# Kernel optimization log

Hardware: AMD Instinct MI355X
Metric: run time of the kernel (lower is better)

## Reference

```python
import jax, jax.numpy as jnp
import numpy as np

ALPHA, BETA, LMBD, GAMMA = 0.0005, 1.0, 1.0, 1.0
MARGIN, THRES = 100.0, 0.5
EPS = 1e-7


def _bce(p, t):
    p = jnp.clip(p, EPS, 1.0 - EPS)
    return -jnp.mean(t * jnp.log(p) + (1.0 - t) * jnp.log1p(-p))


def setup_inputs() -> dict:
    key = jax.random.key(0)
    ks = jax.random.split(key, 9)
    B, T, D, C = 16, 2048, 2048, 100
    return {
        "score_act": jax.random.uniform(ks[0], (B, C), jnp.float32),
        "score_bkg": jax.random.uniform(ks[1], (B, C), jnp.float32),
        "feat_act": jax.random.normal(ks[2], (B, T, D), jnp.float32),
        "feat_bkg": jax.random.normal(ks[3], (B, T, D), jnp.float32),
        "label": jax.random.uniform(ks[4], (B, C), jnp.float32),
        "gt": jax.random.uniform(ks[5], (B, T, C), jnp.float32),
        "sup_cas": jax.random.uniform(ks[6], (B, T, C), jnp.float32),
        "cas_s": jax.random.uniform(ks[7], (B, T, C), jnp.float32),
        "cas_t": jax.random.uniform(ks[8], (B, T, C), jnp.float32),
    }


def reference(score_act, score_bkg, feat_act, feat_bkg, label, gt, sup_cas, cas_s, cas_t):
    # classification BCE against normalized multi-label target
    label_n = label / jnp.sum(label, axis=1, keepdims=True)
    loss_cls = _bce(score_act, label_n)

    # background BCE against uniform 1/C target
    C = label.shape[1]
    loss_be = _bce(score_bkg, jnp.full_like(label, 1.0 / C))

    # uncertainty modeling: feature-magnitude margin loss
    act_norm = jnp.linalg.norm(jnp.mean(feat_act, axis=1), axis=1)  # [B]
    bkg_norm = jnp.linalg.norm(jnp.mean(feat_bkg, axis=1), axis=1)  # [B]
    loss_act = jnp.maximum(MARGIN - act_norm, 0.0)
    loss_um = jnp.mean((loss_act + bkg_norm) ** 2)

    # balanced_ce, vectorized over (batch, class): mean of L2 norms over time
    # for (i,j) slices that contain at least one positive snippet
    pmask = (gt > THRES).astype(sup_cas.dtype)            # [B,T,C]
    norms = jnp.linalg.norm(sup_cas - pmask, axis=1)      # [B,C]
    valid = jnp.sum(pmask, axis=1) > 0                    # [B,C]
    count = jnp.maximum(jnp.sum(valid), 1).astype(norms.dtype)
    loss_sup = jnp.sum(jnp.where(valid, norms, 0.0)) / count

    # student/teacher CAS MSE
    loss_st = jnp.mean((cas_s - cas_t) ** 2)

    loss_total = (loss_cls + ALPHA * loss_um + BETA * loss_be
                  + LMBD * loss_sup + GAMMA * loss_st)
    return jnp.stack([loss_total, loss_cls, loss_be, loss_um, loss_sup, loss_st])
```

## Files before the change

kernel.cpp:

```cpp
#include <hip/hip_runtime.h>
#include <cmath>

constexpr int B = 16, T = 2048, D = 2048, C = 100;
#define EPS_F 1e-7f

__global__ void colsum_kernel(const float* __restrict__ feat, float* __restrict__ out,
                              int rows_per_chunk) {
    const int b = blockIdx.z;
    const int d0 = (blockIdx.x * blockDim.x + threadIdx.x) * 4;
    const int t0 = blockIdx.y * rows_per_chunk;
    float4 acc = make_float4(0.f, 0.f, 0.f, 0.f);
    const float* base = feat + ((size_t)b * T + t0) * D + d0;
    for (int t = 0; t < rows_per_chunk; ++t) {
        float4 v = *reinterpret_cast<const float4*>(base + (size_t)t * D);
        acc.x += v.x; acc.y += v.y; acc.z += v.z; acc.w += v.w;
    }
    float* o = out + b * D + d0;
    atomicAdd(o + 0, acc.x);
    atomicAdd(o + 1, acc.y);
    atomicAdd(o + 2, acc.z);
    atomicAdd(o + 3, acc.w);
}

__global__ void sup_kernel(const float* __restrict__ gt, const float* __restrict__ sup,
                           float* __restrict__ sumsq, float* __restrict__ cnt,
                           int rows_per_chunk) {
    const int b = blockIdx.y;
    const int c = threadIdx.x;
    const int t0 = blockIdx.x * rows_per_chunk;
    if (c >= C) return;
    float acc = 0.f, pc = 0.f;
    size_t base = ((size_t)b * T + t0) * C + c;
    for (int t = 0; t < rows_per_chunk; ++t) {
        float g = gt[base + (size_t)t * C];
        float s = sup[base + (size_t)t * C];
        float m = (g > 0.5f) ? 1.f : 0.f;
        float d = s - m;
        acc += d * d;
        pc += m;
    }
    atomicAdd(&sumsq[b * C + c], acc);
    atomicAdd(&cnt[b * C + c], pc);
}

__global__ void st_kernel(const float4* __restrict__ s, const float4* __restrict__ t,
                          float* __restrict__ acc, int n4) {
    int idx = blockIdx.x * blockDim.x + threadIdx.x;
    int stride = gridDim.x * blockDim.x;
    float local = 0.f;
    for (int i = idx; i < n4; i += stride) {
        float4 a = s[i], b4 = t[i];
        float dx = a.x - b4.x, dy = a.y - b4.y, dz = a.z - b4.z, dw = a.w - b4.w;
        local += dx * dx + dy * dy + dz * dz + dw * dw;
    }
    for (int off = 32; off; off >>= 1) local += __shfl_down(local, off, 64);
    __shared__ float wsum[4];
    int lane = threadIdx.x & 63, wv = threadIdx.x >> 6;
    if (lane == 0) wsum[wv] = local;
    __syncthreads();
    if (threadIdx.x == 0) {
        atomicAdd(acc, wsum[0] + wsum[1] + wsum[2] + wsum[3]);
    }
}

__device__ __forceinline__ float block_reduce256(float v, float* sdata) {
    int tid = threadIdx.x;
    sdata[tid] = v;
    __syncthreads();
    for (int s = 128; s > 0; s >>= 1) {
        if (tid < s) sdata[tid] += sdata[tid + s];
        __syncthreads();
    }
    float r = sdata[0];
    __syncthreads();
    return r;
}

__global__ void final_kernel(const float* __restrict__ score_act,
                             const float* __restrict__ score_bkg,
                             const float* __restrict__ label,
                             const float* __restrict__ colsum_act,
                             const float* __restrict__ colsum_bkg,
                             const float* __restrict__ sup_sumsq,
                             const float* __restrict__ sup_cnt,
                             const float* __restrict__ st_acc,
                             float* __restrict__ out) {
    __shared__ float sdata[256];
    __shared__ float rowsum[B];
    __shared__ float an[B], bn[B];
    const int tid = threadIdx.x;
    const int N = B * C;

    if (tid < B) rowsum[tid] = 0.f;
    __syncthreads();
    for (int i = tid; i < N; i += 256) atomicAdd(&rowsum[i / C], label[i]);
    __syncthreads();

    float lc = 0.f;
    for (int i = tid; i < N; i += 256) {
        float tgt = label[i] / rowsum[i / C];
        float p = fminf(fmaxf(score_act[i], EPS_F), 1.f - EPS_F);
        lc -= tgt * logf(p) + (1.f - tgt) * log1pf(-p);
    }
    float loss_cls = block_reduce256(lc, sdata) / (float)N;

    float lb = 0.f;
    const float u = 1.f / (float)C;
    for (int i = tid; i < N; i += 256) {
        float p = fminf(fmaxf(score_bkg[i], EPS_F), 1.f - EPS_F);
        lb -= u * logf(p) + (1.f - u) * log1pf(-p);
    }
    float loss_be = block_reduce256(lb, sdata) / (float)N;

    const float invT = 1.f / (float)T;
    for (int b = 0; b < B; ++b) {
        float la = 0.f, lg = 0.f;
        for (int d = tid; d < D; d += 256) {
            float va = colsum_act[b * D + d] * invT;
            float vb = colsum_bkg[b * D + d] * invT;
            la += va * va;
            lg += vb * vb;
        }
        float sa = block_reduce256(la, sdata);
        float sb = block_reduce256(lg, sdata);
        if (tid == 0) { an[b] = sqrtf(sa); bn[b] = sqrtf(sb); }
    }
    __syncthreads();

    float ss = 0.f, sc = 0.f;
    for (int i = tid; i < N; i += 256) {
        if (sup_cnt[i] > 0.f) { ss += sqrtf(sup_sumsq[i]); sc += 1.f; }
    }
    float sup_sum = block_reduce256(ss, sdata);
    float sup_count = block_reduce256(sc, sdata);

    if (tid == 0) {
        float loss_um = 0.f;
        for (int b = 0; b < B; ++b) {
            float la = fmaxf(100.f - an[b], 0.f);
            float v = la + bn[b];
            loss_um += v * v;
        }
        loss_um /= (float)B;
        float loss_sup = sup_sum / fmaxf(sup_count, 1.f);
        float loss_st = *st_acc / (float)((size_t)B * T * C);
        float total = loss_cls + 0.0005f * loss_um + 1.0f * loss_be
                    + 1.0f * loss_sup + 1.0f * loss_st;
        out[0] = total;
        out[1] = loss_cls;
        out[2] = loss_be;
        out[3] = loss_um;
        out[4] = loss_sup;
        out[5] = loss_st;
    }
}

extern "C" void kernel_launch(void* const* d_in, const int* in_sizes, int n_in,
                              void* d_out, int out_size, void* d_ws, size_t ws_size,
                              hipStream_t stream) {
    const float* score_act = (const float*)d_in[0];
    const float* score_bkg = (const float*)d_in[1];
    const float* feat_act  = (const float*)d_in[2];
    const float* feat_bkg  = (const float*)d_in[3];
    const float* label     = (const float*)d_in[4];
    const float* gt        = (const float*)d_in[5];
    const float* sup_cas   = (const float*)d_in[6];
    const float* cas_s     = (const float*)d_in[7];
    const float* cas_t     = (const float*)d_in[8];
    float* out = (float*)d_out;
    float* ws  = (float*)d_ws;

    float* colsum_act = ws;
    float* colsum_bkg = ws + (size_t)B * D;
    float* sup_sumsq  = ws + (size_t)2 * B * D;
    float* sup_cnt    = sup_sumsq + B * C;
    float* st_acc     = sup_cnt + B * C;
    size_t ws_needed  = ((size_t)2 * B * D + 2 * B * C + 1) * sizeof(float);

    hipMemsetAsync(d_ws, 0, ws_needed, stream);

    {
        const int rows = 64;
        dim3 grid(D / (256 * 4), T / rows, B);
        colsum_kernel<<<grid, 256, 0, stream>>>(feat_act, colsum_act, rows);
        colsum_kernel<<<grid, 256, 0, stream>>>(feat_bkg, colsum_bkg, rows);
    }
    {
        const int rows = 32;
        dim3 grid(T / rows, B);
        sup_kernel<<<grid, 128, 0, stream>>>(gt, sup_cas, sup_sumsq, sup_cnt, rows);
    }
    {
        int n4 = (B * T * C) / 4;
        st_kernel<<<1024, 256, 0, stream>>>((const float4*)cas_s, (const float4*)cas_t,
                                            st_acc, n4);
    }
    final_kernel<<<1, 256, 0, stream>>>(score_act, score_bkg, label,
                                        colsum_act, colsum_bkg,
                                        sup_sumsq, sup_cnt, st_acc, out);
}
```

Baseline: 664.5 us.

## Fuse colsum launches, merge sup and MSE passes, move norms to parallel kernel

Both feature tensors are now column-summed in one launch that writes per-chunk partials instead of using global atomics. The balanced-CE and student/teacher MSE passes are fused into one kernel that reads all four [B,T,C] tensors in a single sweep, accumulating per-class sums with shared-memory atomics. A new 32-block kernel reduces the partials and computes the feature norms, replacing the serial per-batch loop in the single-block final kernel. The aims are fewer launches, less global atomic contention and a shorter serial tail. In exchange, per-class shared atomics add contention and more partial data has to be written and read back.

```diff
diff --git a/kernel.cpp b/kernel.cpp
--- a/kernel.cpp
+++ b/kernel.cpp
@@ -2,65 +2,28 @@
 #include <cmath>
 
 constexpr int B = 16, T = 2048, D = 2048, C = 100;
+constexpr int NCHUNK = 16;
+constexpr int ROWS = T / NCHUNK;
+constexpr int TCH = 64;
 #define EPS_F 1e-7f
 
-__global__ void colsum_kernel(const float* __restrict__ feat, float* __restrict__ out,
-                              int rows_per_chunk) {
-    const int b = blockIdx.z;
+__global__ void colsum_kernel(const float* __restrict__ feat_act,
+                              const float* __restrict__ feat_bkg,
+                              float* __restrict__ partials) {
+    const int z = blockIdx.z;
+    const int tensor = z >> 4;
+    const int b = z & (B - 1);
+    const int chunk = blockIdx.y;
     const int d0 = (blockIdx.x * blockDim.x + threadIdx.x) * 4;
-    const int t0 = blockIdx.y * rows_per_chunk;
+    const float* __restrict__ feat = tensor ? feat_bkg : feat_act;
+    const float* base = feat + ((size_t)b * T + (size_t)chunk * ROWS) * D + d0;
     float4 acc = make_float4(0.f, 0.f, 0.f, 0.f);
-    const float* base = feat + ((size_t)b * T + t0) * D + d0;
-    for (int t = 0; t < rows_per_chunk; ++t) {
+    for (int t = 0; t < ROWS; ++t) {
         float4 v = *reinterpret_cast<const float4*>(base + (size_t)t * D);
         acc.x += v.x; acc.y += v.y; acc.z += v.z; acc.w += v.w;
     }
-    float* o = out + b * D + d0;
-    atomicAdd(o + 0, acc.x);
-    atomicAdd(o + 1, acc.y);
-    atomicAdd(o + 2, acc.z);
-    atomicAdd(o + 3, acc.w);
-}
-
-__global__ void sup_kernel(const float* __restrict__ gt, const float* __restrict__ sup,
-                           float* __restrict__ sumsq, float* __restrict__ cnt,
-                           int rows_per_chunk) {
-    const int b = blockIdx.y;
-    const int c = threadIdx.x;
-    const int t0 = blockIdx.x * rows_per_chunk;
-    if (c >= C) return;
-    float acc = 0.f, pc = 0.f;
-    size_t base = ((size_t)b * T + t0) * C + c;
-    for (int t = 0; t < rows_per_chunk; ++t) {
-        float g = gt[base + (size_t)t * C];
-        float s = sup[base + (size_t)t * C];
-        float m = (g > 0.5f) ? 1.f : 0.f;
-        float d = s - m;
-        acc += d * d;
-        pc += m;
-    }
-    atomicAdd(&sumsq[b * C + c], acc);
-    atomicAdd(&cnt[b * C + c], pc);
-}
-
-__global__ void st_kernel(const float4* __restrict__ s, const float4* __restrict__ t,
-                          float* __restrict__ acc, int n4) {
-    int idx = blockIdx.x * blockDim.x + threadIdx.x;
-    int stride = gridDim.x * blockDim.x;
-    float local = 0.f;
-    for (int i = idx; i < n4; i += stride) {
-        float4 a = s[i], b4 = t[i];
-        float dx = a.x - b4.x, dy = a.y - b4.y, dz = a.z - b4.z, dw = a.w - b4.w;
-        local += dx * dx + dy * dy + dz * dz + dw * dw;
-    }
-    for (int off = 32; off; off >>= 1) local += __shfl_down(local, off, 64);
-    __shared__ float wsum[4];
-    int lane = threadIdx.x & 63, wv = threadIdx.x >> 6;
-    if (lane == 0) wsum[wv] = local;
-    __syncthreads();
-    if (threadIdx.x == 0) {
-        atomicAdd(acc, wsum[0] + wsum[1] + wsum[2] + wsum[3]);
-    }
+    float* o = partials + (((size_t)tensor * NCHUNK + chunk) * B + b) * D + d0;
+    *reinterpret_cast<float4*>(o) = acc;
 }
 
 __device__ __forceinline__ float block_reduce256(float v, float* sdata) {
@@ -76,18 +39,84 @@
     return r;
 }
 
+__global__ void btc_kernel(const float* __restrict__ gt,
+                           const float* __restrict__ sup,
+                           const float* __restrict__ cs,
+                           const float* __restrict__ ct,
+                           float* __restrict__ sup_sumsq,
+                           float* __restrict__ sup_cnt,
+                           float* __restrict__ st_acc) {
+    __shared__ float s_ss[C];
+    __shared__ float s_cn[C];
+    __shared__ float wsum[4];
+    const int b = blockIdx.y;
+    const int t0 = blockIdx.x * TCH;
+    const int tid = threadIdx.x;
+    if (tid < C) { s_ss[tid] = 0.f; s_cn[tid] = 0.f; }
+    __syncthreads();
+
+    const size_t base = ((size_t)b * T + t0) * C;
+    float st_local = 0.f;
+    for (int i = tid; i < TCH * C; i += 256) {
+        size_t idx = base + i;
+        float g = gt[idx];
+        float s = sup[idx];
+        float a = cs[idx];
+        float t = ct[idx];
+        float m = (g > 0.5f) ? 1.f : 0.f;
+        float d = s - m;
+        int c = i % C;
+        atomicAdd(&s_ss[c], d * d);
+        atomicAdd(&s_cn[c], m);
+        float e = a - t;
+        st_local += e * e;
+    }
+    for (int off = 32; off; off >>= 1) st_local += __shfl_down(st_local, off, 64);
+    int lane = tid & 63, wv = tid >> 6;
+    if (lane == 0) wsum[wv] = st_local;
+    __syncthreads();
+    if (tid < C) {
+        atomicAdd(&sup_sumsq[b * C + tid], s_ss[tid]);
+        atomicAdd(&sup_cnt[b * C + tid], s_cn[tid]);
+    }
+    if (tid == 0) {
+        atomicAdd(st_acc, wsum[0] + wsum[1] + wsum[2] + wsum[3]);
+    }
+}
+
+__global__ void norm_kernel(const float* __restrict__ partials,
+                            float* __restrict__ norms) {
+    __shared__ float sdata[256];
+    const int z = blockIdx.x;
+    const int tensor = z >> 4;
+    const int b = z & (B - 1);
+    const int tid = threadIdx.x;
+    const float invT = 1.f / (float)T;
+    float acc = 0.f;
+    for (int d0 = tid * 4; d0 < D; d0 += 1024) {
+        float4 s = make_float4(0.f, 0.f, 0.f, 0.f);
+        for (int ch = 0; ch < NCHUNK; ++ch) {
+            const float4 v = *reinterpret_cast<const float4*>(
+                partials + (((size_t)tensor * NCHUNK + ch) * B + b) * D + d0);
+            s.x += v.x; s.y += v.y; s.z += v.z; s.w += v.w;
+        }
+        float mx = s.x * invT, my = s.y * invT, mz = s.z * invT, mw = s.w * invT;
+        acc += mx * mx + my * my + mz * mz + mw * mw;
+    }
+    float total = block_reduce256(acc, sdata);
+    if (tid == 0) norms[z] = sqrtf(total);
+}
+
 __global__ void final_kernel(const float* __restrict__ score_act,
                              const float* __restrict__ score_bkg,
                              const float* __restrict__ label,
-                             const float* __restrict__ colsum_act,
-                             const float* __restrict__ colsum_bkg,
+                             const float* __restrict__ norms,
                              const float* __restrict__ sup_sumsq,
                              const float* __restrict__ sup_cnt,
                              const float* __restrict__ st_acc,
                              float* __restrict__ out) {
     __shared__ float sdata[256];
     __shared__ float rowsum[B];
-    __shared__ float an[B], bn[B];
     const int tid = threadIdx.x;
     const int N = B * C;
 
@@ -112,21 +141,6 @@
     }
     float loss_be = block_reduce256(lb, sdata) / (float)N;
 
-    const float invT = 1.f / (float)T;
-    for (int b = 0; b < B; ++b) {
-        float la = 0.f, lg = 0.f;
-        for (int d = tid; d < D; d += 256) {
-            float va = colsum_act[b * D + d] * invT;
-            float vb = colsum_bkg[b * D + d] * invT;
-            la += va * va;
-            lg += vb * vb;
-        }
-        float sa = block_reduce256(la, sdata);
-        float sb = block_reduce256(lg, sdata);
-        if (tid == 0) { an[b] = sqrtf(sa); bn[b] = sqrtf(sb); }
-    }
-    __syncthreads();
-
     float ss = 0.f, sc = 0.f;
     for (int i = tid; i < N; i += 256) {
         if (sup_cnt[i] > 0.f) { ss += sqrtf(sup_sumsq[i]); sc += 1.f; }
@@ -137,8 +151,10 @@
     if (tid == 0) {
         float loss_um = 0.f;
         for (int b = 0; b < B; ++b) {
-            float la = fmaxf(100.f - an[b], 0.f);
-            float v = la + bn[b];
+            float an = norms[b];
+            float bn = norms[B + b];
+            float la = fmaxf(100.f - an, 0.f);
+            float v = la + bn;
             loss_um += v * v;
         }
         loss_um /= (float)B;
@@ -170,32 +186,25 @@
     float* out = (float*)d_out;
     float* ws  = (float*)d_ws;
 
-    float* colsum_act = ws;
-    float* colsum_bkg = ws + (size_t)B * D;
-    float* sup_sumsq  = ws + (size_t)2 * B * D;
-    float* sup_cnt    = sup_sumsq + B * C;
-    float* st_acc     = sup_cnt + B * C;
-    size_t ws_needed  = ((size_t)2 * B * D + 2 * B * C + 1) * sizeof(float);
-
-    hipMemsetAsync(d_ws, 0, ws_needed, stream);
+    float* sup_sumsq = ws;
+    float* sup_cnt   = ws + 1600;
+    float* st_acc    = ws + 3200;
+    float* norms     = ws + 3216;
+    float* partials  = ws + 4096;
+
+    hipMemsetAsync(d_ws, 0, 3201 * sizeof(float), stream);
 
     {
-        const int rows = 64;
-        dim3 grid(D / (256 * 4), T / rows, B);
-        colsum_kernel<<<grid, 256, 0, stream>>>(feat_act, colsum_act, rows);
-        colsum_kernel<<<grid, 256, 0, stream>>>(feat_bkg, colsum_bkg, rows);
+        dim3 grid(D / (256 * 4), NCHUNK, 2 * B);
+        colsum_kernel<<<grid, 256, 0, stream>>>(feat_act, feat_bkg, partials);
     }
     {
-        const int rows = 32;
-        dim3 grid(T / rows, B);
-        sup_kernel<<<grid, 128, 0, stream>>>(gt, sup_cas, sup_sumsq, sup_cnt, rows);
-    }
-    {
-        int n4 = (B * T * C) / 4;
-        st_kernel<<<1024, 256, 0, stream>>>((const float4*)cas_s, (const float4*)cas_t,
-                                            st_acc, n4);
-    }
-    final_kernel<<<1, 256, 0, stream>>>(score_act, score_bkg, label,
-                                        colsum_act, colsum_bkg,
+        dim3 grid(T / TCH, B);
+        btc_kernel<<<grid, 256, 0, stream>>>(gt, sup_cas, cas_s, cas_t,
+                                             sup_sumsq, sup_cnt, st_acc);
+    }
+    norm_kernel<<<dim3(2 * B), 256, 0, stream>>>(partials, norms);
+
+    final_kernel<<<1, 256, 0, stream>>>(score_act, score_bkg, label, norms,
                                         sup_sumsq, sup_cnt, st_acc, out);
 }
```

Result: faster. 604.6 us (-9.0%).
